# Kernel tuning notes

Hardware: AMD Instinct MI355X
Metric: run time of the kernel (lower is better)

Reference implementation:

```python
import jax, jax.numpy as jnp
import numpy as np

K = 3          # hypergraph neighbors (hardcoded self.kn = 3)
H = 3          # attention heads (hardcoded num_heads=3)
QKD = 32       # qkv_dim
BN_EPS = 1e-5


def _pe(channels, num_frames):
    # Ter_Embed: sinusoidal over frame index, constant across joints -> (1,C,T,1)
    pos = jnp.arange(num_frames, dtype=jnp.float32)
    div = jnp.exp(jnp.arange(0, channels, 2, dtype=jnp.float32) * (-np.log(10000.0) / channels))
    ang = pos[:, None] * div[None, :]                      # (T, C/2)
    pe = jnp.zeros((num_frames, channels), jnp.float32)
    pe = pe.at[:, 0::2].set(jnp.sin(ang)).at[:, 1::2].set(jnp.cos(ang))
    return pe.T[None, :, :, None]                          # (1,C,T,1)


def _bn(x, g, b):
    # training-mode BatchNorm2d over (N,T,V) per channel
    mu = x.mean(axis=(0, 2, 3), keepdims=True)
    var = x.var(axis=(0, 2, 3), keepdims=True)
    return (x - mu) * jax.lax.rsqrt(var + BN_EPS) * g[None, :, None, None] + b[None, :, None, None]


def setup_inputs() -> dict:
    key = jax.random.key(0)
    ks = jax.random.split(key, 16)
    N, C, T, V = 8, 128, 64, 204
    s = 0.05
    inp = {
        'x': jax.random.normal(ks[0], (N, C, T, V), jnp.float32),
        # Transform.conv1: Conv1d(k, k*k, C, groups=k) -> weight (k*k, 1, C)
        'trans_w': jax.random.normal(ks[1], (K * K, C), jnp.float32) * s,
        'trans_b': jax.random.normal(ks[2], (K * K,), jnp.float32) * s,
        # VertexConv.convK1: Conv1d(k, 1, 1)
        'convk_w': jax.random.normal(ks[3], (K,), jnp.float32) * s,
        'convk_b': jax.random.normal(ks[4], (1,), jnp.float32) * s,
        # to_qkvs: Conv2d(C, 2*H*QKD, 1)
        'qkv_w': jax.random.normal(ks[5], (2 * H * QKD, C), jnp.float32) * s,
        'qkv_b': jax.random.normal(ks[6], (2 * H * QKD,), jnp.float32) * s,
        'alphas': jnp.ones((1, H, 1, 1), jnp.float32),
        'att1s': jnp.broadcast_to(jnp.eye(T, dtype=jnp.float32), (1, H, T, T)) + 0.0,
        # out_nets: Conv2d(H*C, C, (1,1)) + BN
        'out_w': jax.random.normal(ks[7], (C, H * C), jnp.float32) * s,
        'out_b': jax.random.normal(ks[8], (C,), jnp.float32) * s,
        'out_g': jnp.ones((C,), jnp.float32) + jax.random.normal(ks[9], (C,), jnp.float32) * 0.01,
        'out_beta': jax.random.normal(ks[10], (C,), jnp.float32) * 0.01,
        # ff_net: Conv2d(C, C, 1) + BN
        'ff_w': jax.random.normal(ks[11], (C, C), jnp.float32) * s,
        'ff_b': jax.random.normal(ks[12], (C,), jnp.float32) * s,
        'ff_g': jnp.ones((C,), jnp.float32) + jax.random.normal(ks[13], (C,), jnp.float32) * 0.01,
        'ff_beta': jax.random.normal(ks[14], (C,), jnp.float32) * 0.01,
    }
    return inp


def reference(x, trans_w, trans_b, convk_w, convk_b, qkv_w, qkv_b, alphas, att1s,
              out_w, out_b, out_g, out_beta, ff_w, ff_b, ff_g, ff_beta):
    N, C, T, V = x.shape
    orign = x
    # ---------- hypergraph_knn (ssa) ----------
    # cos_dis: F.normalize over last dim (V) then contract c,t -> (N,V,V)
    nrm = jnp.linalg.norm(x, axis=-1, keepdims=True)
    xn = x / jnp.maximum(nrm, 1e-12)
    dis = jnp.einsum('nctu,nctv->nuv', xn, xn)
    _, idx = jax.lax.top_k(dis, K)                                   # (N,V,K)
    # gather neighbor feats: feats[n,c,t,v,k] = x[n,c,t,idx[n,v,k]]
    feats = jnp.take_along_axis(x[:, :, :, None, :], idx[:, None, None, :, :], axis=4)  # (N,C,T,V,K)
    # Transform: grouped Conv1d over C, group g -> K outputs
    m = feats.mean(axis=2).transpose(0, 2, 3, 1)                     # (N,V,K,C)
    mult = jnp.einsum('nvgc,gpc->nvgp', m, trans_w.reshape(K, K, C)) + trans_b.reshape(K, K)
    mult = jax.nn.softmax(mult, axis=-1)                             # (N,V,K,K)
    transformed = jnp.einsum('nctvk,nvkp->nctvp', feats, mult)
    # convK1 pools K -> 1
    pooled = jnp.einsum('nctvk,k->nctv', transformed, convk_w) + convk_b[0]
    x = jax.nn.relu(pooled + orign)
    # ---------- TTA_Block_att ----------
    xs = x + _pe(C, T)
    qkv = jnp.einsum('oc,nctv->notv', qkv_w, xs) + qkv_b[None, :, None, None]
    qkv = qkv.reshape(N, 2 * H, QKD, T, V)
    q, k = qkv[:, :H], qkv[:, H:]
    att = jnp.tanh(jnp.einsum('nhctv,nhcqv->nhtq', q, k) / (QKD * V)) * alphas + att1s  # (N,H,T,T)
    xs2 = jnp.einsum('nctv,nstq->nscqv', x, att).reshape(N, H * C, T, V)
    out = jnp.einsum('os,nstv->notv', out_w, xs2) + out_b[None, :, None, None]
    out = _bn(out, out_g, out_beta)
    xs3 = jax.nn.leaky_relu(out + x, 0.1)                            # ress is identity (in==out)
    ff = jnp.einsum('oc,nctv->notv', ff_w, xs3) + ff_b[None, :, None, None]
    ff = _bn(ff, ff_g, ff_beta)
    return jax.nn.leaky_relu(ff + x, 0.1)
```

## Files before the change

kernel.cpp:

```cpp
#include <hip/hip_runtime.h>
#include <math.h>

#define N_ 8
#define C_ 128
#define T_ 64
#define V_ 204
#define H_ 3
#define QKD_ 32
#define O2_ 192
#define TV_ 13056
#define CT_ 8192
#define TT_ 4096
#define VV_ 41616
#define NCTV_ 13369344ull
#define DSPLIT_ 16
#define ZR_ 208

typedef __attribute__((ext_vector_type(8))) short short8v;
typedef __attribute__((ext_vector_type(4))) float f32x4;

__device__ inline unsigned short bf16rnd(float f) {
  union { float f; unsigned u; } x; x.f = f;
  return (unsigned short)((x.u + 0x7FFFu + ((x.u >> 16) & 1u)) >> 16);
}
__device__ inline float bf2f(unsigned short u) {
  union { unsigned u; float f; } x; x.u = ((unsigned)u) << 16;
  return x.f;
}

__global__ void k_wprep(const float* __restrict__ qw, const float* __restrict__ ow,
                        const float* __restrict__ fw, unsigned short* __restrict__ wb) {
  int g = blockIdx.x * 256 + threadIdx.x;
  if (g >= 704 * 16) return;
  int row = g >> 4, ch = g & 15;
  const float* src;
  if (row < 192) src = qw + row * 128;
  else if (row < 576) { int r = row - 192; src = ow + (r & 127) * 384 + (r >> 7) * 128; }
  else src = fw + (row - 576) * 128;
  f32x4 a = *(const f32x4*)(src + ch * 8);
  f32x4 b = *(const f32x4*)(src + ch * 8 + 4);
  unsigned short buf[8];
  buf[0] = bf16rnd(a.x); buf[1] = bf16rnd(a.y); buf[2] = bf16rnd(a.z); buf[3] = bf16rnd(a.w);
  buf[4] = bf16rnd(b.x); buf[5] = bf16rnd(b.y); buf[6] = bf16rnd(b.z); buf[7] = bf16rnd(b.w);
  *(uint4*)(wb + (size_t)row * 128 + ch * 8) = *(const uint4*)buf;
}

__global__ void k_qkvpe(const float* __restrict__ qw, const float* __restrict__ qb,
                        float* __restrict__ qpe) {
  __shared__ float pes[C_ * T_];
  int tid = threadIdx.x;
  for (int i = tid; i < C_ * T_; i += 256) {
    int t = i & 63, c = i >> 6;
    int j = c >> 1;
    float dv = expf((2.0f * j) * (-logf(10000.0f) / (float)C_));
    float ang = (float)t * dv;
    pes[i] = (c & 1) ? cosf(ang) : sinf(ang);
  }
  __syncthreads();
  int g = blockIdx.x * 256 + tid;
  int t = g & 63, m = g >> 6;
  float a = 0.f;
  for (int c = 0; c < C_; ++c) a += qw[m * C_ + c] * pes[c * T_ + t];
  qpe[g] = a + qb[m];
}

__global__ void k_scale(const float* __restrict__ x, float* __restrict__ s) {
  int gid = blockIdx.x * blockDim.x + threadIdx.x;
  int w = gid >> 6, lane = gid & 63;
  if (w >= N_ * CT_) return;
  const f32x4* row = (const f32x4*)(x + (size_t)w * V_);
  float a = 0.f;
  for (int v4 = lane; v4 < 51; v4 += 64) {
    f32x4 t = row[v4];
    a += t.x * t.x + t.y * t.y + t.z * t.z + t.w * t.w;
  }
#pragma unroll
  for (int off = 32; off >= 1; off >>= 1) a += __shfl_down(a, off, 64);
  if (lane == 0) {
    float d = fmaxf(sqrtf(a), 1e-12f);
    s[w] = 1.0f / (d * d);
  }
}

__global__ __launch_bounds__(256) void k_zprep(const float* __restrict__ x,
                                               const float* __restrict__ s,
                                               unsigned short* __restrict__ zhi,
                                               unsigned short* __restrict__ zlo,
                                               float* __restrict__ cm) {
  int kt = blockIdx.x, ut = blockIdx.y, n = blockIdx.z;
  int k0 = kt * 64, u0 = ut * 64;
  __shared__ float Ts[64][65];
  __shared__ float sq[64];
  int tid = threadIdx.x;
  int uu = tid & 63, kk = tid >> 6;
  int u = u0 + uu;
  bool uok = u < V_;
  const float* xb = x + (size_t)n * CT_ * V_;
#pragma unroll
  for (int it = 0; it < 16; ++it) {
    int kr = kk + it * 4;
    Ts[kr][uu] = uok ? xb[(size_t)(k0 + kr) * V_ + u] : 0.f;
  }
  if (tid < 64) sq[tid] = sqrtf(s[(size_t)n * CT_ + k0 + tid]);
  __syncthreads();
  if (tid < 64 && uok) {
    float a = 0.f;
    for (int t = 0; t < 64; ++t) a += Ts[t][tid];
    cm[((size_t)n * C_ + kt) * V_ + u] = a * (1.0f / 64.0f);
  }
#pragma unroll
  for (int it = 0; it < 4; ++it) {
    int sl = tid + it * 256;
    int u_l = sl & 63, oct = (sl >> 6) & 7, half = sl >> 9;
    int ug = u0 + u_l;
    if (ug >= ZR_) continue;
    unsigned short buf[8];
    if (ug < V_) {
#pragma unroll
      for (int j = 0; j < 8; ++j) {
        float z = Ts[oct * 8 + j][u_l] * sq[oct * 8 + j];
        unsigned short h = bf16rnd(z);
        buf[j] = half ? bf16rnd(z - bf2f(h)) : h;
      }
    } else {
#pragma unroll
      for (int j = 0; j < 8; ++j) buf[j] = 0;
    }
    unsigned short* dst = (half ? zlo : zhi) +
                          (((size_t)n * 1024 + kt * 8 + oct) * ZR_ + ug) * 8;
    *(uint4*)dst = *(const uint4*)buf;
  }
}

__global__ __launch_bounds__(256) void k_dism(const unsigned short* __restrict__ zhi,
                                              const unsigned short* __restrict__ zlo,
                                              float* __restrict__ pdis) {
  int q = blockIdx.x, sp = blockIdx.y, n = blockIdx.z;
  int bu = (q == 2) ? 1 : 0, bv = (q == 0) ? 0 : 1;
  int u0 = bu * 128, v0 = bv * 128;
  bool dg = (bu == bv);
  __shared__ unsigned short As[8 * 128 * 8];
  __shared__ unsigned short Bs[8 * 128 * 8];
  int tid = threadIdx.x, lane = tid & 63, wid = tid >> 6;
  int lr = lane & 15, lg = lane >> 4;
  f32x4 acc[2][8];
#pragma unroll
  for (int mi = 0; mi < 2; ++mi)
#pragma unroll
    for (int li = 0; li < 8; ++li) acc[mi][li] = (f32x4){0.f, 0.f, 0.f, 0.f};
  int kend = sp * 512 + 512;
  for (int kk = sp * 512; kk < kend; kk += 32) {
    int koct = kk >> 3;
    __syncthreads();
#pragma unroll
    for (int it = 0; it < 4; ++it) {
      int sl = tid + it * 256;
      int row = sl & 127, hs = sl >> 7;
      int slot = hs & 3, half = hs >> 2;
      const unsigned short* src = half ? zlo : zhi;
      size_t ob = ((size_t)n * 1024 + koct + slot) * ZR_;
      int ra = u0 + row; ra = ra > 207 ? 207 : ra;
      *(uint4*)&As[(hs * 128 + row) * 8] = *(const uint4*)(src + (ob + ra) * 8);
      if (!dg) {
        int rb = v0 + row; rb = rb > 207 ? 207 : rb;
        *(uint4*)&Bs[(hs * 128 + row) * 8] = *(const uint4*)(src + (ob + rb) * 8);
      }
    }
    __syncthreads();
    const unsigned short* Bp = dg ? As : Bs;
    short8v ah[2], al[2];
#pragma unroll
    for (int mi = 0; mi < 2; ++mi) {
      int r = wid * 32 + mi * 16 + lr;
      ah[mi] = *(const short8v*)&As[(lg * 128 + r) * 8];
      al[mi] = *(const short8v*)&As[((4 + lg) * 128 + r) * 8];
    }
#pragma unroll
    for (int li = 0; li < 8; ++li) {
      int rv = li * 16 + lr;
      short8v bh = *(const short8v*)&Bp[(lg * 128 + rv) * 8];
      short8v bl = *(const short8v*)&Bp[((4 + lg) * 128 + rv) * 8];
#pragma unroll
      for (int mi = 0; mi < 2; ++mi) {
        acc[mi][li] = __builtin_amdgcn_mfma_f32_16x16x32_bf16(ah[mi], bh, acc[mi][li], 0, 0, 0);
        acc[mi][li] = __builtin_amdgcn_mfma_f32_16x16x32_bf16(ah[mi], bl, acc[mi][li], 0, 0, 0);
        acc[mi][li] = __builtin_amdgcn_mfma_f32_16x16x32_bf16(al[mi], bh, acc[mi][li], 0, 0, 0);
      }
    }
  }
  float* pb = pdis + ((size_t)sp * N_ + n) * VV_;
#pragma unroll
  for (int mi = 0; mi < 2; ++mi) {
#pragma unroll
    for (int li = 0; li < 8; ++li) {
      int v = v0 + li * 16 + lr;
      if (v >= V_) continue;
#pragma unroll
      for (int rr = 0; rr < 4; ++rr) {
        int u = u0 + wid * 32 + mi * 16 + lg * 4 + rr;
        if (u >= V_) continue;
        float val = acc[mi][li][rr];
        pb[(size_t)u * V_ + v] = val;
        if (!dg) pb[(size_t)v * V_ + u] = val;
      }
    }
  }
}

__global__ void k_topk2(const float* __restrict__ pdis, int* __restrict__ idx) {
  int r = blockIdx.x;
  int n = r / V_, u = r - n * V_;
  int lane = threadIdx.x;
  float m0 = -INFINITY, m1 = -INFINITY, m2 = -INFINITY;
  int i0 = 0x7fffffff, i1 = 0x7fffffff, i2 = 0x7fffffff;
#pragma unroll
  for (int g = 0; g < 4; ++g) {
    int v = g * 64 + lane;
    if (v >= V_) break;
    float a = 0.f;
#pragma unroll
    for (int sp = 0; sp < DSPLIT_; ++sp)
      a += pdis[((size_t)sp * N_ + n) * VV_ + (size_t)u * V_ + v];
    if (a > m0 || (a == m0 && v < i0)) {
      m2 = m1; i2 = i1; m1 = m0; i1 = i0; m0 = a; i0 = v;
    } else if (a > m1 || (a == m1 && v < i1)) {
      m2 = m1; i2 = i1; m1 = a; i1 = v;
    } else if (a > m2 || (a == m2 && v < i2)) {
      m2 = a; i2 = v;
    }
  }
#pragma unroll
  for (int msk = 1; msk < 64; msk <<= 1) {
    float o0 = __shfl_xor(m0, msk, 64), o1 = __shfl_xor(m1, msk, 64),
          o2 = __shfl_xor(m2, msk, 64);
    int p0 = __shfl_xor(i0, msk, 64), p1 = __shfl_xor(i1, msk, 64),
        p2 = __shfl_xor(i2, msk, 64);
    float ov[3] = {o0, o1, o2};
    int op[3] = {p0, p1, p2};
#pragma unroll
    for (int e = 0; e < 3; ++e) {
      float a = ov[e]; int v = op[e];
      if (a > m0 || (a == m0 && v < i0)) {
        m2 = m1; i2 = i1; m1 = m0; i1 = i0; m0 = a; i0 = v;
      } else if (a > m1 || (a == m1 && v < i1)) {
        m2 = m1; i2 = i1; m1 = a; i1 = v;
      } else if (a > m2 || (a == m2 && v < i2)) {
        m2 = a; i2 = v;
      }
    }
  }
  if (lane == 0) {
    idx[r * 3 + 0] = i0; idx[r * 3 + 1] = i1; idx[r * 3 + 2] = i2;
  }
}

__global__ void k_w2(const float* __restrict__ cm, const int* __restrict__ idx,
                     const float* __restrict__ tw, const float* __restrict__ tb,
                     const float* __restrict__ ckw, float* __restrict__ w2) {
  int r = blockIdx.x;
  int n = r / V_;
  int lane = threadIdx.x;
  __shared__ float mv[3][C_];
  const int* ib = idx + r * 3;
  int j0 = ib[0], j1 = ib[1], j2 = ib[2];
  const float* cmn = cm + (size_t)n * C_ * V_;
  for (int c = lane; c < C_; c += 64) {
    mv[0][c] = cmn[c * V_ + j0];
    mv[1][c] = cmn[c * V_ + j1];
    mv[2][c] = cmn[c * V_ + j2];
  }
  __syncthreads();
  float p[9];
#pragma unroll
  for (int gp = 0; gp < 9; ++gp) p[gp] = 0.f;
  for (int c = lane; c < C_; c += 64) {
#pragma unroll
    for (int g = 0; g < 3; ++g) {
      float m = mv[g][c];
#pragma unroll
      for (int pp = 0; pp < 3; ++pp) p[g * 3 + pp] += m * tw[(g * 3 + pp) * C_ + c];
    }
  }
#pragma unroll
  for (int off = 32; off >= 1; off >>= 1) {
#pragma unroll
    for (int gp = 0; gp < 9; ++gp) p[gp] += __shfl_down(p[gp], off, 64);
  }
  if (lane == 0) {
    float c0 = ckw[0], c1 = ckw[1], c2 = ckw[2];
#pragma unroll
    for (int g = 0; g < 3; ++g) {
      float m0 = p[g * 3 + 0] + tb[g * 3 + 0];
      float m1 = p[g * 3 + 1] + tb[g * 3 + 1];
      float m2 = p[g * 3 + 2] + tb[g * 3 + 2];
      float mx = fmaxf(m0, fmaxf(m1, m2));
      float e0 = expf(m0 - mx), e1 = expf(m1 - mx), e2 = expf(m2 - mx);
      float inv = 1.0f / (e0 + e1 + e2);
      w2[r * 3 + g] = (e0 * c0 + e1 * c1 + e2 * c2) * inv;
    }
  }
}

__global__ __launch_bounds__(256) void k_x1p(const float* __restrict__ x,
                                             const int* __restrict__ idx,
                                             const float* __restrict__ w2,
                                             const float* __restrict__ ckb,
                                             float* __restrict__ x1p,
                                             unsigned short* __restrict__ x1pb) {
  int t = blockIdx.x, ct = blockIdx.y, n = blockIdx.z;
  int c0 = ct * 32;
  __shared__ float Ts[32][209];
  __shared__ int iw[V_ * 3];
  __shared__ float ww[V_ * 3];
  int tid = threadIdx.x;
  const float* xb = x + ((size_t)n * C_ + c0) * TV_ + t * V_;
  for (int i = tid; i < 32 * V_; i += 256) {
    int c = i / V_, v = i - c * V_;
    Ts[c][v] = xb[(size_t)c * TV_ + v];
  }
  for (int i = tid; i < V_ * 3; i += 256) {
    iw[i] = idx[(size_t)n * V_ * 3 + i];
    ww[i] = w2[(size_t)n * V_ * 3 + i];
  }
  __syncthreads();
  float cb = ckb[0];
  for (int i = tid; i < 32 * V_; i += 256) {
    int v = i >> 5, cl = i & 31;
    int b = v * 3;
    float pooled = Ts[cl][iw[b]] * ww[b] + Ts[cl][iw[b + 1]] * ww[b + 1] +
                   Ts[cl][iw[b + 2]] * ww[b + 2] + cb;
    float val = fmaxf(pooled + Ts[cl][v], 0.f);
    size_t o = ((size_t)(n * V_ + v) * T_ + t) * C_ + c0 + cl;
    x1p[o] = val;
    x1pb[o] = bf16rnd(val);
  }
}

template <int MCH, int OBF>
__global__ __launch_bounds__(256) void k_gmm2(const unsigned short* __restrict__ Wb,
                                              const unsigned short* __restrict__ Xp,
                                              const float* __restrict__ addv,
                                              void* __restrict__ Yv) {
  int l0 = blockIdx.x * 128, n = blockIdx.z;
  __shared__ unsigned short Xs[128 * 136];
  __shared__ unsigned short Ys[64 * 128];
  int tid = threadIdx.x, lane = tid & 63, wid = tid >> 6;
  int wm = wid >> 1, wl = wid & 1;
  int lr = lane & 15, lg = lane >> 4;
  const unsigned short* xb = Xp + ((size_t)n * TV_ + l0) * 128;
#pragma unroll
  for (int it = 0; it < 8; ++it) {
    int g = tid + it * 256;
    int row = g >> 4, ch = g & 15;
    *(uint4*)&Xs[row * 136 + ch * 8] = *(const uint4*)(xb + (size_t)row * 128 + ch * 8);
  }
  __syncthreads();
  for (int mc = 0; mc < MCH; ++mc) {
    short8v a[2][4];
#pragma unroll
    for (int mi = 0; mi < 2; ++mi) {
      int m = mc * 64 + wm * 32 + mi * 16 + lr;
#pragma unroll
      for (int ks = 0; ks < 4; ++ks)
        a[mi][ks] = *(const short8v*)(Wb + (size_t)m * 128 + ks * 32 + lg * 8);
    }
    f32x4 acc[2][4];
#pragma unroll
    for (int mi = 0; mi < 2; ++mi)
#pragma unroll
      for (int li = 0; li < 4; ++li) acc[mi][li] = (f32x4){0.f, 0.f, 0.f, 0.f};
#pragma unroll
    for (int ks = 0; ks < 4; ++ks) {
#pragma unroll
      for (int li = 0; li < 4; ++li) {
        short8v b = *(const short8v*)&Xs[(wl * 64 + li * 16 + lr) * 136 + ks * 32 + lg * 8];
#pragma unroll
        for (int mi = 0; mi < 2; ++mi)
          acc[mi][li] = __builtin_amdgcn_mfma_f32_16x16x32_bf16(a[mi][ks], b, acc[mi][li], 0, 0, 0);
      }
    }
    if (OBF) {
      __syncthreads();
#pragma unroll
      for (int mi = 0; mi < 2; ++mi)
#pragma unroll
        for (int li = 0; li < 4; ++li) {
          int lloc = wl * 64 + li * 16 + lr;
          int tt = (l0 + lloc) & 63;
#pragma unroll
          for (int r = 0; r < 4; ++r) {
            int mloc = wm * 32 + mi * 16 + lg * 4 + r;
            float val = acc[mi][li][r] + addv[(mc * 64 + mloc) * 64 + tt];
            Ys[mloc * 128 + lloc] = bf16rnd(val);
          }
        }
      __syncthreads();
      unsigned short* Yh = (unsigned short*)Yv;
#pragma unroll
      for (int it = 0; it < 4; ++it) {
        int g = tid + it * 256;
        int row = g >> 4, ch = g & 15;
        *(uint4*)(Yh + ((size_t)n * O2_ + mc * 64 + row) * TV_ + l0 + ch * 8) =
            *(const uint4*)&Ys[row * 128 + ch * 8];
      }
    } else {
      float* Yf = (float*)Yv;
#pragma unroll
      for (int mi = 0; mi < 2; ++mi)
#pragma unroll
        for (int li = 0; li < 4; ++li) {
          int lp = l0 + wl * 64 + li * 16 + lr;
          int m = mc * 64 + wm * 32 + mi * 16 + lg * 4;
          f32x4 o;
#pragma unroll
          for (int r = 0; r < 4; ++r) o[r] = acc[mi][li][r] + addv[m + r];
          *(f32x4*)(Yf + ((size_t)n * TV_ + lp) * 128 + m) = o;
        }
    }
  }
}

__global__ __launch_bounds__(256) void k_att(const unsigned short* __restrict__ qkv,
                                             float* __restrict__ attp) {
  int cp = blockIdx.x, h = blockIdx.y, n = blockIdx.z;
  __shared__ float Qs[102][68], Ks[102][68];
  int tid = threadIdx.x;
  int ty = tid >> 4, tx = tid & 15;
  float acc[4][4] = {};
  for (int cc = 0; cc < 2; ++cc) {
    int c = cp * 2 + cc;
    const unsigned short* qb = qkv + ((size_t)n * O2_ + h * QKD_ + c) * TV_;
    const unsigned short* kb = qkv + ((size_t)n * O2_ + H_ * QKD_ + h * QKD_ + c) * TV_;
    for (int vh = 0; vh < 2; ++vh) {
      for (int g = tid; g < 816; g += 256) {
        int v = g >> 3, t0 = (g & 7) * 8;
        uint4 qv = *(const uint4*)(qb + vh * 6528 + g * 8);
        uint4 kv = *(const uint4*)(kb + vh * 6528 + g * 8);
        const unsigned short* qs = (const unsigned short*)&qv;
        const unsigned short* ks2 = (const unsigned short*)&kv;
#pragma unroll
        for (int j = 0; j < 8; ++j) {
          Qs[v][t0 + j] = bf2f(qs[j]);
          Ks[v][t0 + j] = bf2f(ks2[j]);
        }
      }
      __syncthreads();
      for (int vv = 0; vv < 102; ++vv) {
        f32x4 qa = *(const f32x4*)&Qs[vv][ty * 4];
        f32x4 ka = *(const f32x4*)&Ks[vv][tx * 4];
#pragma unroll
        for (int i = 0; i < 4; ++i)
#pragma unroll
          for (int j = 0; j < 4; ++j) acc[i][j] += qa[i] * ka[j];
      }
      __syncthreads();
    }
  }
  float* ar = attp + (((size_t)cp * N_ + n) * H_ + h) * TT_;
#pragma unroll
  for (int i = 0; i < 4; ++i)
#pragma unroll
    for (int j = 0; j < 4; ++j)
      ar[(ty * 4 + i) * T_ + tx * 4 + j] = acc[i][j];
}

__global__ void k_attfin(const float* __restrict__ attp, const float* __restrict__ alphas,
                         const float* __restrict__ att1s, unsigned short* __restrict__ attT) {
  int i = blockIdx.x * blockDim.x + threadIdx.x;
  if (i >= N_ * H_ * TT_) return;
  int tt = i % TT_;
  int h = (i / TT_) % H_;
  int n = i / (H_ * TT_);
  float raw = 0.f;
#pragma unroll
  for (int cp = 0; cp < 16; ++cp)
    raw += attp[(((size_t)cp * N_ + n) * H_ + h) * TT_ + tt];
  int t = tt >> 6, q = tt & 63;
  float v = tanhf(raw * (1.0f / 6528.0f)) * alphas[h] + att1s[h * TT_ + tt];
  attT[(size_t)(n * 64 + q) * 192 + h * 64 + t] = bf16rnd(v);
}

__global__ __launch_bounds__(256) void k_fcomb(const unsigned short* __restrict__ x1pb,
                                               const unsigned short* __restrict__ w3b,
                                               const unsigned short* __restrict__ attT,
                                               const float* __restrict__ outb,
                                               float* __restrict__ op) {
  int v = blockIdx.x, n = blockIdx.z;
  __shared__ unsigned short Xv[64 * 136];
  __shared__ unsigned short Yv[128 * 72];
  int tid = threadIdx.x, lane = tid & 63, wid = tid >> 6;
  int lr = lane & 15, lg = lane >> 4;
  const unsigned short* xb = x1pb + ((size_t)(n * V_ + v) * T_) * 128;
#pragma unroll
  for (int it = 0; it < 4; ++it) {
    int g = tid + it * 256;
    int row = g >> 4, ch = g & 15;
    *(uint4*)&Xv[row * 136 + ch * 8] = *(const uint4*)(xb + (size_t)row * 128 + ch * 8);
  }
  __syncthreads();
  f32x4 acc2[4][2];
#pragma unroll
  for (int mq = 0; mq < 4; ++mq)
#pragma unroll
    for (int oi = 0; oi < 2; ++oi) acc2[mq][oi] = (f32x4){0.f, 0.f, 0.f, 0.f};
  const unsigned short* ab = attT + (size_t)n * 64 * 192;
  for (int h = 0; h < H_; ++h) {
    short8v a1[2][4];
#pragma unroll
    for (int mi = 0; mi < 2; ++mi) {
      int m = wid * 32 + mi * 16 + lr;
#pragma unroll
      for (int ks = 0; ks < 4; ++ks)
        a1[mi][ks] = *(const short8v*)(w3b + ((size_t)(h * 128 + m)) * 128 + ks * 32 + lg * 8);
    }
    f32x4 acc1[2][4];
#pragma unroll
    for (int mi = 0; mi < 2; ++mi)
#pragma unroll
      for (int li = 0; li < 4; ++li) acc1[mi][li] = (f32x4){0.f, 0.f, 0.f, 0.f};
#pragma unroll
    for (int ks = 0; ks < 4; ++ks) {
#pragma unroll
      for (int li = 0; li < 4; ++li) {
        short8v b = *(const short8v*)&Xv[(li * 16 + lr) * 136 + ks * 32 + lg * 8];
#pragma unroll
        for (int mi = 0; mi < 2; ++mi)
          acc1[mi][li] = __builtin_amdgcn_mfma_f32_16x16x32_bf16(a1[mi][ks], b, acc1[mi][li], 0, 0, 0);
      }
    }
    __syncthreads();
#pragma unroll
    for (int mi = 0; mi < 2; ++mi)
#pragma unroll
      for (int li = 0; li < 4; ++li) {
        int t = li * 16 + lr;
#pragma unroll
        for (int r = 0; r < 4; ++r) {
          int o = wid * 32 + mi * 16 + lg * 4 + r;
          Yv[o * 72 + t] = bf16rnd(acc1[mi][li][r]);
        }
      }
    __syncthreads();
#pragma unroll
    for (int ks2 = 0; ks2 < 2; ++ks2) {
      short8v bY[2];
#pragma unroll
      for (int oi = 0; oi < 2; ++oi)
        bY[oi] = *(const short8v*)&Yv[(wid * 32 + oi * 16 + lr) * 72 + ks2 * 32 + lg * 8];
#pragma unroll
      for (int mq = 0; mq < 4; ++mq) {
        short8v a2 = *(const short8v*)(ab + (size_t)(mq * 16 + lr) * 192 + h * 64 + ks2 * 32 + lg * 8);
#pragma unroll
        for (int oi = 0; oi < 2; ++oi)
          acc2[mq][oi] = __builtin_amdgcn_mfma_f32_16x16x32_bf16(a2, bY[oi], acc2[mq][oi], 0, 0, 0);
      }
    }
  }
#pragma unroll
  for (int mq = 0; mq < 4; ++mq)
#pragma unroll
    for (int oi = 0; oi < 2; ++oi) {
      int o = wid * 32 + oi * 16 + lr;
      float bo = outb[o];
#pragma unroll
      for (int r = 0; r < 4; ++r) {
        int q = mq * 16 + lg * 4 + r;
        op[((size_t)(n * V_ + v) * T_ + q) * 128 + o] = acc2[mq][oi][r] + bo;
      }
    }
}

__global__ void k_bnstats_p(const float* __restrict__ xp, float* __restrict__ part) {
  int blk = blockIdx.x;
  int tid = threadIdx.x;
  int c4 = tid & 31, rg = tid >> 5;
  const f32x4* x4 = (const f32x4*)xp;
  size_t base = (size_t)blk * 512;
  f32x4 s1 = {0.f, 0.f, 0.f, 0.f}, s2 = {0.f, 0.f, 0.f, 0.f};
  for (int r = rg; r < 512; r += 8) {
    f32x4 val = x4[(base + r) * 32 + c4];
#pragma unroll
    for (int j = 0; j < 4; ++j) { s1[j] += val[j]; s2[j] += val[j] * val[j]; }
  }
  __shared__ f32x4 red1[8][32], red2[8][32];
  red1[rg][c4] = s1; red2[rg][c4] = s2;
  __syncthreads();
  if (tid < 32) {
    f32x4 a1 = red1[0][tid], a2 = red2[0][tid];
#pragma unroll
    for (int g = 1; g < 8; ++g) {
#pragma unroll
      for (int j = 0; j < 4; ++j) { a1[j] += red1[g][tid][j]; a2[j] += red2[g][tid][j]; }
    }
    *(f32x4*)(part + blk * 256 + tid * 4) = a1;
    *(f32x4*)(part + blk * 256 + 128 + tid * 4) = a2;
  }
}

__global__ void k_bnab(const float* __restrict__ part, const float* __restrict__ g,
                       const float* __restrict__ beta, float* __restrict__ ab) {
  int c = threadIdx.x;
  float s1 = 0.f, s2 = 0.f;
  for (int b = 0; b < 204; ++b) {
    s1 += part[b * 256 + c];
    s2 += part[b * 256 + 128 + c];
  }
  const float cnt = (float)(N_ * TV_);
  float mu = s1 / cnt;
  float rstd = rsqrtf(s2 / cnt - mu * mu + 1e-5f);
  float a = rstd * g[c];
  ab[c] = a;
  ab[128 + c] = beta[c] - mu * a;
}

__global__ void k_bnxt(const float* __restrict__ op, const float* __restrict__ x1p,
                       const float* __restrict__ ab, unsigned short* __restrict__ xt) {
  __shared__ float sa[128], sb[128];
  int tid = threadIdx.x;
  if (tid < 128) { sa[tid] = ab[tid]; sb[tid] = ab[128 + tid]; }
  __syncthreads();
  const unsigned NU = (unsigned)(NCTV_ / 8);
  const f32x4* o4 = (const f32x4*)op;
  const f32x4* r4 = (const f32x4*)x1p;
  for (unsigned u = blockIdx.x * 256u + tid; u < NU; u += gridDim.x * 256u) {
    unsigned row = u >> 4, ch = u & 15;
    unsigned bi = row * 32 + ch * 2;
    f32x4 v0 = o4[bi], v1 = o4[bi + 1];
    f32x4 q0 = r4[bi], q1 = r4[bi + 1];
    int c8 = ch * 8;
    unsigned short buf[8];
#pragma unroll
    for (int j = 0; j < 4; ++j) {
      float t0 = v0[j] * sa[c8 + j] + sb[c8 + j] + q0[j];
      float t1 = v1[j] * sa[c8 + 4 + j] + sb[c8 + 4 + j] + q1[j];
      buf[j] = bf16rnd(t0 > 0.f ? t0 : 0.1f * t0);
      buf[4 + j] = bf16rnd(t1 > 0.f ? t1 : 0.1f * t1);
    }
    *(uint4*)(xt + (size_t)u * 8) = *(const uint4*)buf;
  }
}

__global__ __launch_bounds__(256) void k_bnfinal(const float* __restrict__ ff,
                                                 const float* __restrict__ x1p,
                                                 const float* __restrict__ ab,
                                                 float* __restrict__ dout) {
  int ct = blockIdx.x, t = blockIdx.y, n = blockIdx.z;
  int c0 = ct * 32;
  __shared__ float Tf[V_][33];
  __shared__ float sa[32], sb[32];
  int tid = threadIdx.x;
  if (tid < 32) { sa[tid] = ab[c0 + tid]; sb[tid] = ab[128 + c0 + tid]; }
  __syncthreads();
  for (int i = tid; i < V_ * 32; i += 256) {
    int v = i >> 5, cl = i & 31;
    size_t a = ((size_t)(n * V_ + v) * T_ + t) * 128 + c0 + cl;
    float val = ff[a] * sa[cl] + sb[cl] + x1p[a];
    Tf[v][cl] = val > 0.f ? val : 0.1f * val;
  }
  __syncthreads();
  for (int i = tid; i < 32 * V_; i += 256) {
    int cl = i / V_, v = i - cl * V_;
    dout[((size_t)(n * C_ + c0 + cl) * T_ + t) * V_ + v] = Tf[v][cl];
  }
}

extern "C" void kernel_launch(void* const* d_in, const int* in_sizes, int n_in,
                              void* d_out, int out_size, void* d_ws, size_t ws_size,
                              hipStream_t stream) {
  (void)in_sizes; (void)n_in; (void)out_size; (void)ws_size;
  const float* x        = (const float*)d_in[0];
  const float* trans_w  = (const float*)d_in[1];
  const float* trans_b  = (const float*)d_in[2];
  const float* convk_w  = (const float*)d_in[3];
  const float* convk_b  = (const float*)d_in[4];
  const float* qkv_w    = (const float*)d_in[5];
  const float* qkv_b    = (const float*)d_in[6];
  const float* alphas   = (const float*)d_in[7];
  const float* att1s    = (const float*)d_in[8];
  const float* out_w    = (const float*)d_in[9];
  const float* out_b    = (const float*)d_in[10];
  const float* out_g    = (const float*)d_in[11];
  const float* out_beta = (const float*)d_in[12];
  const float* ff_w     = (const float*)d_in[13];
  const float* ff_b     = (const float*)d_in[14];
  const float* ff_g     = (const float*)d_in[15];
  const float* ff_beta  = (const float*)d_in[16];

  float* ws = (float*)d_ws;
  size_t off = 0;
  float* x1p  = ws + off; off += NCTV_;
  float* big  = ws + off; off += (size_t)N_ * O2_ * TV_ / 2;
  float* pre  = ws + off; off += NCTV_;
  float* sbuf = ws + off; off += (size_t)N_ * CT_;
  int*   idx  = (int*)(ws + off); off += (size_t)N_ * V_ * 3 + 4;
  float* cm   = ws + off; off += (size_t)N_ * C_ * V_;
  float* w2   = ws + off; off += (size_t)N_ * V_ * 3 + 4;
  float* attp = ws + off; off += (size_t)16 * N_ * H_ * TT_;
  unsigned short* attT = (unsigned short*)(ws + off); off += (size_t)N_ * 64 * 192 / 2;
  float* part = ws + off; off += 204 * 256;
  float* ab   = ws + off; off += 512;
  float* qpe  = ws + off; off += (size_t)O2_ * T_;
  unsigned short* wb = (unsigned short*)(ws + off); off += 704 * 128 / 2;
  const size_t ZEL = (size_t)N_ * 1024 * ZR_ * 8;
  unsigned short* zhi = (unsigned short*)(ws + off);
  unsigned short* zlo = zhi + ZEL;
  off += ZEL;
  unsigned short* x1pb  = zhi;
  unsigned short* xs3pb = zlo;
  unsigned short* qkvb  = (unsigned short*)big;
  float* dout = (float*)d_out;

  k_wprep<<<44, 256, 0, stream>>>(qkv_w, out_w, ff_w, wb);
  k_qkvpe<<<48, 256, 0, stream>>>(qkv_w, qkv_b, qpe);
  k_scale<<<(N_ * CT_ * 64) / 256, 256, 0, stream>>>(x, sbuf);
  k_zprep<<<dim3(128, 4, N_), 256, 0, stream>>>(x, sbuf, zhi, zlo, cm);
  k_dism<<<dim3(3, DSPLIT_, N_), 256, 0, stream>>>(zhi, zlo, big);
  k_topk2<<<N_ * V_, 64, 0, stream>>>(big, idx);
  k_w2<<<N_ * V_, 64, 0, stream>>>(cm, idx, trans_w, trans_b, convk_w, w2);
  k_x1p<<<dim3(64, 4, N_), 256, 0, stream>>>(x, idx, w2, convk_b, x1p, x1pb);

  k_gmm2<3, 1><<<dim3(102, 1, N_), 256, 0, stream>>>(wb, x1pb, qpe, qkvb);
  k_att<<<dim3(16, H_, N_), 256, 0, stream>>>(qkvb, attp);
  k_attfin<<<384, 256, 0, stream>>>(attp, alphas, att1s, attT);

  k_fcomb<<<dim3(204, 1, N_), 256, 0, stream>>>(x1pb, wb + 192 * 128, attT, out_b, pre);

  k_bnstats_p<<<204, 256, 0, stream>>>(pre, part);
  k_bnab<<<1, 128, 0, stream>>>(part, out_g, out_beta, ab);
  k_bnxt<<<2048, 256, 0, stream>>>(pre, x1p, ab, xs3pb);

  k_gmm2<2, 0><<<dim3(102, 1, N_), 256, 0, stream>>>(wb + 576 * 128, xs3pb, ff_b, pre);
  k_bnstats_p<<<204, 256, 0, stream>>>(pre, part);
  k_bnab<<<1, 128, 0, stream>>>(part, ff_g, ff_beta, ab + 256);
  k_bnfinal<<<dim3(4, 64, N_), 256, 0, stream>>>(pre, x1p, ab + 256, dout);
}
```

Measured before the change: 382.6 us.

## Fuse BatchNorm statistics into GEMM epilogues and parallelize BN finalize

Per-channel sum and sum-of-squares for both BatchNorms are now computed inside the fcomb and ff GEMM epilogues using wave shuffles. This removes the two separate stats passes that re-read the full pre-activation tensor. The finalize kernel becomes a 128-block tree reduction over 1632 partials instead of one 128-thread block looping serially. fcomb also drops its LDS staging of X and reads B fragments straight from global memory, the distance GEMM split doubles to 32 along K, and its partial output goes to the larger `pre` buffer. The risks are more partials to reduce, uncoalesced global fragment reads in fcomb, and more atomic-free partial traffic in the topk input.

```diff
diff --git a/kernel.cpp b/kernel.cpp
--- a/kernel.cpp
+++ b/kernel.cpp
@@ -13,8 +13,9 @@
 #define TT_ 4096
 #define VV_ 41616
 #define NCTV_ 13369344ull
-#define DSPLIT_ 16
+#define DSPLIT_ 32
 #define ZR_ 208
+#define NBLK_ 1632
 
 typedef __attribute__((ext_vector_type(8))) short short8v;
 typedef __attribute__((ext_vector_type(4))) float f32x4;
@@ -148,8 +149,9 @@
   for (int mi = 0; mi < 2; ++mi)
 #pragma unroll
     for (int li = 0; li < 8; ++li) acc[mi][li] = (f32x4){0.f, 0.f, 0.f, 0.f};
-  int kend = sp * 512 + 512;
-  for (int kk = sp * 512; kk < kend; kk += 32) {
+  const int KCH = CT_ / DSPLIT_;
+  int kbase = sp * KCH, kend = kbase + KCH;
+  for (int kk = kbase; kk < kend; kk += 32) {
     int koct = kk >> 3;
     __syncthreads();
 #pragma unroll
@@ -336,11 +338,12 @@
   }
 }
 
-template <int MCH, int OBF>
+template <int MCH, int OBF, int STATS>
 __global__ __launch_bounds__(256) void k_gmm2(const unsigned short* __restrict__ Wb,
                                               const unsigned short* __restrict__ Xp,
                                               const float* __restrict__ addv,
-                                              void* __restrict__ Yv) {
+                                              void* __restrict__ Yv,
+                                              float* __restrict__ part) {
   int l0 = blockIdx.x * 128, n = blockIdx.z;
   __shared__ unsigned short Xs[128 * 136];
   __shared__ unsigned short Ys[64 * 128];
@@ -405,6 +408,7 @@
       }
     } else {
       float* Yf = (float*)Yv;
+      float st1[2][4] = {}, st2[2][4] = {};
 #pragma unroll
       for (int mi = 0; mi < 2; ++mi)
 #pragma unroll
@@ -413,9 +417,30 @@
           int m = mc * 64 + wm * 32 + mi * 16 + lg * 4;
           f32x4 o;
 #pragma unroll
-          for (int r = 0; r < 4; ++r) o[r] = acc[mi][li][r] + addv[m + r];
+          for (int r = 0; r < 4; ++r) {
+            o[r] = acc[mi][li][r] + addv[m + r];
+            if (STATS) { st1[mi][r] += o[r]; st2[mi][r] += o[r] * o[r]; }
+          }
           *(f32x4*)(Yf + ((size_t)n * TV_ + lp) * 128 + m) = o;
         }
+      if (STATS) {
+        int blk2 = ((n * gridDim.x + blockIdx.x) * 2 + wl) * 256;
+#pragma unroll
+        for (int mi = 0; mi < 2; ++mi)
+#pragma unroll
+          for (int r = 0; r < 4; ++r) {
+            float a1 = st1[mi][r], a2 = st2[mi][r];
+            a1 += __shfl_xor(a1, 1, 64); a2 += __shfl_xor(a2, 1, 64);
+            a1 += __shfl_xor(a1, 2, 64); a2 += __shfl_xor(a2, 2, 64);
+            a1 += __shfl_xor(a1, 4, 64); a2 += __shfl_xor(a2, 4, 64);
+            a1 += __shfl_xor(a1, 8, 64); a2 += __shfl_xor(a2, 8, 64);
+            if (lr == 0) {
+              int m = mc * 64 + wm * 32 + mi * 16 + lg * 4 + r;
+              part[blk2 + m] = a1;
+              part[blk2 + 128 + m] = a2;
+            }
+          }
+      }
     }
   }
 }
@@ -484,20 +509,13 @@
                                                const unsigned short* __restrict__ w3b,
                                                const unsigned short* __restrict__ attT,
                                                const float* __restrict__ outb,
-                                               float* __restrict__ op) {
+                                               float* __restrict__ op,
+                                               float* __restrict__ part) {
   int v = blockIdx.x, n = blockIdx.z;
-  __shared__ unsigned short Xv[64 * 136];
   __shared__ unsigned short Yv[128 * 72];
   int tid = threadIdx.x, lane = tid & 63, wid = tid >> 6;
   int lr = lane & 15, lg = lane >> 4;
   const unsigned short* xb = x1pb + ((size_t)(n * V_ + v) * T_) * 128;
-#pragma unroll
-  for (int it = 0; it < 4; ++it) {
-    int g = tid + it * 256;
-    int row = g >> 4, ch = g & 15;
-    *(uint4*)&Xv[row * 136 + ch * 8] = *(const uint4*)(xb + (size_t)row * 128 + ch * 8);
-  }
-  __syncthreads();
   f32x4 acc2[4][2];
 #pragma unroll
   for (int mq = 0; mq < 4; ++mq)
@@ -522,7 +540,7 @@
     for (int ks = 0; ks < 4; ++ks) {
 #pragma unroll
       for (int li = 0; li < 4; ++li) {
-        short8v b = *(const short8v*)&Xv[(li * 16 + lr) * 136 + ks * 32 + lg * 8];
+        short8v b = *(const short8v*)(xb + (size_t)(li * 16 + lr) * 128 + ks * 32 + lg * 8);
 #pragma unroll
         for (int mi = 0; mi < 2; ++mi)
           acc1[mi][li] = __builtin_amdgcn_mfma_f32_16x16x32_bf16(a1[mi][ks], b, acc1[mi][li], 0, 0, 0);
@@ -556,6 +574,7 @@
       }
     }
   }
+  float s1[2] = {0.f, 0.f}, s2[2] = {0.f, 0.f};
 #pragma unroll
   for (int mq = 0; mq < 4; ++mq)
 #pragma unroll
@@ -565,52 +584,49 @@
 #pragma unroll
       for (int r = 0; r < 4; ++r) {
         int q = mq * 16 + lg * 4 + r;
-        op[((size_t)(n * V_ + v) * T_ + q) * 128 + o] = acc2[mq][oi][r] + bo;
-      }
-    }
-}
-
-__global__ void k_bnstats_p(const float* __restrict__ xp, float* __restrict__ part) {
-  int blk = blockIdx.x;
-  int tid = threadIdx.x;
-  int c4 = tid & 31, rg = tid >> 5;
-  const f32x4* x4 = (const f32x4*)xp;
-  size_t base = (size_t)blk * 512;
-  f32x4 s1 = {0.f, 0.f, 0.f, 0.f}, s2 = {0.f, 0.f, 0.f, 0.f};
-  for (int r = rg; r < 512; r += 8) {
-    f32x4 val = x4[(base + r) * 32 + c4];
-#pragma unroll
-    for (int j = 0; j < 4; ++j) { s1[j] += val[j]; s2[j] += val[j] * val[j]; }
-  }
-  __shared__ f32x4 red1[8][32], red2[8][32];
-  red1[rg][c4] = s1; red2[rg][c4] = s2;
-  __syncthreads();
-  if (tid < 32) {
-    f32x4 a1 = red1[0][tid], a2 = red2[0][tid];
-#pragma unroll
-    for (int g = 1; g < 8; ++g) {
-#pragma unroll
-      for (int j = 0; j < 4; ++j) { a1[j] += red1[g][tid][j]; a2[j] += red2[g][tid][j]; }
-    }
-    *(f32x4*)(part + blk * 256 + tid * 4) = a1;
-    *(f32x4*)(part + blk * 256 + 128 + tid * 4) = a2;
+        float val = acc2[mq][oi][r] + bo;
+        op[((size_t)(n * V_ + v) * T_ + q) * 128 + o] = val;
+        s1[oi] += val; s2[oi] += val * val;
+      }
+    }
+  int blk = (n * V_ + v) * 256;
+#pragma unroll
+  for (int oi = 0; oi < 2; ++oi) {
+    float a1 = s1[oi], a2 = s2[oi];
+    a1 += __shfl_xor(a1, 16, 64); a2 += __shfl_xor(a2, 16, 64);
+    a1 += __shfl_xor(a1, 32, 64); a2 += __shfl_xor(a2, 32, 64);
+    if ((lane & 48) == 0) {
+      int o = wid * 32 + oi * 16 + lr;
+      part[blk + o] = a1;
+      part[blk + 128 + o] = a2;
+    }
   }
 }
 
 __global__ void k_bnab(const float* __restrict__ part, const float* __restrict__ g,
                        const float* __restrict__ beta, float* __restrict__ ab) {
-  int c = threadIdx.x;
+  int c = blockIdx.x;
+  int tid = threadIdx.x;
   float s1 = 0.f, s2 = 0.f;
-  for (int b = 0; b < 204; ++b) {
+  for (int b = tid; b < NBLK_; b += 256) {
     s1 += part[b * 256 + c];
     s2 += part[b * 256 + 128 + c];
   }
-  const float cnt = (float)(N_ * TV_);
-  float mu = s1 / cnt;
-  float rstd = rsqrtf(s2 / cnt - mu * mu + 1e-5f);
-  float a = rstd * g[c];
-  ab[c] = a;
-  ab[128 + c] = beta[c] - mu * a;
+  __shared__ float r1[256], r2[256];
+  r1[tid] = s1; r2[tid] = s2;
+  __syncthreads();
+  for (int off = 128; off >= 1; off >>= 1) {
+    if (tid < off) { r1[tid] += r1[tid + off]; r2[tid] += r2[tid + off]; }
+    __syncthreads();
+  }
+  if (tid == 0) {
+    const float cnt = (float)(N_ * TV_);
+    float mu = r1[0] / cnt;
+    float rstd = rsqrtf(r2[0] / cnt - mu * mu + 1e-5f);
+    float a = rstd * g[c];
+    ab[c] = a;
+    ab[128 + c] = beta[c] - mu * a;
+  }
 }
 
 __global__ void k_bnxt(const float* __restrict__ op, const float* __restrict__ x1p,
@@ -697,7 +713,7 @@
   float* w2   = ws + off; off += (size_t)N_ * V_ * 3 + 4;
   float* attp = ws + off; off += (size_t)16 * N_ * H_ * TT_;
   unsigned short* attT = (unsigned short*)(ws + off); off += (size_t)N_ * 64 * 192 / 2;
-  float* part = ws + off; off += 204 * 256;
+  float* part = ws + off; off += (size_t)NBLK_ * 256;
   float* ab   = ws + off; off += 512;
   float* qpe  = ws + off; off += (size_t)O2_ * T_;
   unsigned short* wb = (unsigned short*)(ws + off); off += 704 * 128 / 2;
@@ -714,23 +730,21 @@
   k_qkvpe<<<48, 256, 0, stream>>>(qkv_w, qkv_b, qpe);
   k_scale<<<(N_ * CT_ * 64) / 256, 256, 0, stream>>>(x, sbuf);
   k_zprep<<<dim3(128, 4, N_), 256, 0, stream>>>(x, sbuf, zhi, zlo, cm);
-  k_dism<<<dim3(3, DSPLIT_, N_), 256, 0, stream>>>(zhi, zlo, big);
-  k_topk2<<<N_ * V_, 64, 0, stream>>>(big, idx);
+  k_dism<<<dim3(3, DSPLIT_, N_), 256, 0, stream>>>(zhi, zlo, pre);
+  k_topk2<<<N_ * V_, 64, 0, stream>>>(pre, idx);
   k_w2<<<N_ * V_, 64, 0, stream>>>(cm, idx, trans_w, trans_b, convk_w, w2);
   k_x1p<<<dim3(64, 4, N_), 256, 0, stream>>>(x, idx, w2, convk_b, x1p, x1pb);
 
-  k_gmm2<3, 1><<<dim3(102, 1, N_), 256, 0, stream>>>(wb, x1pb, qpe, qkvb);
+  k_gmm2<3, 1, 0><<<dim3(102, 1, N_), 256, 0, stream>>>(wb, x1pb, qpe, qkvb, nullptr);
   k_att<<<dim3(16, H_, N_), 256, 0, stream>>>(qkvb, attp);
   k_attfin<<<384, 256, 0, stream>>>(attp, alphas, att1s, attT);
 
-  k_fcomb<<<dim3(204, 1, N_), 256, 0, stream>>>(x1pb, wb + 192 * 128, attT, out_b, pre);
-
-  k_bnstats_p<<<204, 256, 0, stream>>>(pre, part);
-  k_bnab<<<1, 128, 0, stream>>>(part, out_g, out_beta, ab);
+  k_fcomb<<<dim3(204, 1, N_), 256, 0, stream>>>(x1pb, wb + 192 * 128, attT, out_b, pre, part);
+
+  k_bnab<<<128, 256, 0, stream>>>(part, out_g, out_beta, ab);
   k_bnxt<<<2048, 256, 0, stream>>>(pre, x1p, ab, xs3pb);
 
-  k_gmm2<2, 0><<<dim3(102, 1, N_), 256, 0, stream>>>(wb + 576 * 128, xs3pb, ff_b, pre);
-  k_bnstats_p<<<204, 256, 0, stream>>>(pre, part);
-  k_bnab<<<1, 128, 0, stream>>>(part, ff_g, ff_beta, ab + 256);
+  k_gmm2<2, 0, 1><<<dim3(102, 1, N_), 256, 0, stream>>>(wb + 576 * 128, xs3pb, ff_b, pre, part);
+  k_bnab<<<128, 256, 0, stream>>>(part, ff_g, ff_beta, ab + 256);
   k_bnfinal<<<dim3(4, 64, N_), 256, 0, stream>>>(pre, x1p, ab + 256, dout);
 }
```

Measured after the change: 364.1 us. 4.8% less time.
